# Kernel optimization log

Measured on AMD Instinct MI355X. Metric: run time of the kernel, lower is better.

The kernel has to match this reference:

```python
import jax, jax.numpy as jnp
import numpy as np

N_NODES = 50000
N_EDGES = 800000
IN_DIM = 256
HID_DIM = 128
N_LAYERS = 3


def setup_inputs() -> dict:
    key = jax.random.key(0)
    ks = jax.random.split(key, 7)
    s = 0.05
    x = jax.random.normal(ks[0], (N_NODES, IN_DIM), dtype=jnp.float32)
    edge_index = jax.random.randint(ks[1], (2, N_EDGES), 0, N_NODES, dtype=jnp.int64)
    W_enc = jax.random.normal(ks[2], (HID_DIM, IN_DIM), dtype=jnp.float32) * s
    b_enc = jax.random.normal(ks[3], (HID_DIM,), dtype=jnp.float32) * s
    W_l = jax.random.normal(ks[4], (N_LAYERS, HID_DIM, HID_DIM), dtype=jnp.float32) * s
    b_l = jax.random.normal(ks[5], (N_LAYERS, HID_DIM), dtype=jnp.float32) * s
    W_r = jax.random.normal(ks[6], (N_LAYERS, HID_DIM, HID_DIM), dtype=jnp.float32) * s
    return {"x": x, "edge_index": edge_index, "W_enc": W_enc, "b_enc": b_enc,
            "W_l": W_l, "b_l": b_l, "W_r": W_r}


def reference(x, edge_index, W_enc, b_enc, W_l, b_l, W_r):
    # eval mode: dropout is identity
    n = x.shape[0]
    src, dst = edge_index[0], edge_index[1]
    # encode: Linear(in_dim -> hid_dim)
    h = x @ W_enc.T + b_enc  # [N, H]
    # in-degree for mean aggregation (nodes with no in-edges -> 0 output)
    deg = jax.ops.segment_sum(jnp.ones((src.shape[0],), h.dtype), dst, num_segments=n)
    denom = jnp.maximum(deg, 1.0)[:, None]  # [N, 1]
    for i in range(W_l.shape[0]):
        # mean of source-node features over incoming edges
        agg = jax.ops.segment_sum(h[src], dst, num_segments=n) / denom  # [N, H]
        # SAGEConv: lin_l(agg) + lin_r(h)  (lin_r has no bias)
        h = agg @ W_l[i].T + b_l[i] + h @ W_r[i].T
    return h
```

## Files before the change

### kernel.cpp

```cpp
#include <hip/hip_runtime.h>

#define N_NODES 50000
#define N_EDGES 800000
#define IN_DIM 256
#define HID_DIM 128
#define ROWTILES (N_NODES / 16)
#define SCAT_BLOCKS (N_EDGES / 256)
#define ENC_BLOCKS 512
#define WCVT_BLOCKS 48
#define NBLK_LAYER 768
#define CAP_E 352

typedef float f4 __attribute__((ext_vector_type(4)));
typedef float f32x4 __attribute__((ext_vector_type(4)));
typedef float vf2 __attribute__((ext_vector_type(2)));
typedef short bf16x8 __attribute__((ext_vector_type(8)));

__device__ __forceinline__ unsigned short f2bf(float f) {
    unsigned u = __builtin_bit_cast(unsigned, f);
    return (unsigned short)((u + 0x7fffu + ((u >> 16) & 1u)) >> 16);
}
__device__ __forceinline__ unsigned pk2(float a, float b) {
    return (unsigned)f2bf(a) | ((unsigned)f2bf(b) << 16);
}
__device__ __forceinline__ bf16x8 cvt8(f4 a, f4 b) {
    union { bf16x8 v; unsigned u[4]; } r;
    r.u[0] = pk2(a[0], a[1]);
    r.u[1] = pk2(a[2], a[3]);
    r.u[2] = pk2(b[0], b[1]);
    r.u[3] = pk2(b[2], b[3]);
    return r.v;
}
__device__ __forceinline__ vf2 dec8(unsigned short t) {
    return __builtin_amdgcn_cvt_pk_f32_fp8((int)(unsigned)t, false);
}
__device__ __forceinline__ void gl_lds16(const void* g, void* l) {
    __builtin_amdgcn_global_load_lds(
        (const __attribute__((address_space(1))) unsigned int*)g,
        (__attribute__((address_space(3))) unsigned int*)l, 16, 0, 0);
}


__global__ __launch_bounds__(256) void k_pre(const int* __restrict__ src, const int* __restrict__ dst,
                                             int* __restrict__ tcnt16, unsigned* __restrict__ buf,
                                             const float* __restrict__ Wl, const float* __restrict__ Wr,
                                             unsigned short* __restrict__ wlrbf,
                                             const float* __restrict__ x,
                                             const float* __restrict__ Wenc,
                                             const float* __restrict__ bias,
                                             unsigned short* __restrict__ hout,
                                             unsigned char* __restrict__ f8out,
                                             int* __restrict__ ticket) {
    __shared__ float xs[2][4096];
    int tid = threadIdx.x;
    if (blockIdx.x < WCVT_BLOCKS) {
        int idx = blockIdx.x * 2048 + tid * 8;
        const float* srcp = (idx < 49152) ? (Wl + idx) : (Wr + (idx - 49152));
        const f4* g = (const f4*)srcp;
        *(bf16x8*)(wlrbf + idx) = cvt8(g[0], g[1]);
        return;
    }
    if (blockIdx.x >= WCVT_BLOCKS + ENC_BLOCKS) {
        int e = (blockIdx.x - WCVT_BLOCKS - ENC_BLOCKS) * 256 + tid;
        if (e < N_EDGES) {
            int sv = src[e], dv = dst[e];
            int t = dv >> 4, dl = dv & 15;
            int p = atomicAdd(&tcnt16[t * 16], 1);
            if (p < CAP_E) buf[t * CAP_E + p] = (unsigned)sv | ((unsigned)dl << 16);
        }
        return;
    }
    int bid = blockIdx.x - WCVT_BLOCKS;
    int lane = tid & 63;
    int wv = tid >> 6;
    int colbase = wv * 32;
    int lr = lane & 15;
    int kh = (lane >> 4) * 8;
    int khB = kh * 4;
    int swz = (lr & 7) << 4;

    bf16x8 bfr[2][8];
#pragma unroll
    for (int n = 0; n < 2; ++n) {
        const float* wp = Wenc + (size_t)(colbase + n * 16 + lr) * IN_DIM + kh;
#pragma unroll
        for (int s = 0; s < 8; ++s) {
            const f4* g = (const f4*)(wp + s * 32);
            bfr[n][s] = cvt8(g[0], g[1]);
        }
    }
    float bias0 = bias[colbase + lr];
    float bias1 = bias[colbase + 16 + lr];

    int pb = 0;
    for (int rt = bid; rt < ROWTILES; rt += ENC_BLOCKS, pb ^= 1) {
#pragma unroll
        for (int jj = 0; jj < 4; ++jj) {
            int j = wv * 4 + jj;
            const char* gsrc = (const char*)(x + (size_t)(rt * 16 + j) * IN_DIM)
                               + ((lane * 16) ^ ((j & 7) << 4));
            gl_lds16(gsrc, (char*)&xs[pb][0] + j * 1024);
        }
        __syncthreads();

        const char* xb = (const char*)&xs[pb][0] + lr * 1024;
        bf16x8 afr[8];
#pragma unroll
        for (int s = 0; s < 8; ++s) {
            int lo = khB + s * 128;
            f4 a = *(const f4*)(xb + ((lo) ^ swz));
            f4 b = *(const f4*)(xb + ((lo + 16) ^ swz));
            afr[s] = cvt8(a, b);
        }
        f32x4 acc0 = {0.f, 0.f, 0.f, 0.f}, acc1 = {0.f, 0.f, 0.f, 0.f};
#pragma unroll
        for (int s = 0; s < 8; ++s) {
            acc0 = __builtin_amdgcn_mfma_f32_16x16x32_bf16(afr[s], bfr[0][s], acc0, 0, 0, 0);
            acc1 = __builtin_amdgcn_mfma_f32_16x16x32_bf16(afr[s], bfr[1][s], acc1, 0, 0, 0);
        }
        int rbase = rt * 16 + (lane >> 4) * 4;
#pragma unroll
        for (int r = 0; r < 4; ++r) {
            float v0 = acc0[r] + bias0, v1 = acc1[r] + bias1;
            unsigned short* op = hout + (size_t)(rbase + r) * HID_DIM;
            op[colbase + lr] = f2bf(v0);
            op[colbase + 16 + lr] = f2bf(v1);
            unsigned pk = (unsigned)__builtin_amdgcn_cvt_pk_fp8_f32(v0, v1, 0, false);
            unsigned char* fp = f8out + (size_t)(rbase + r) * HID_DIM;
            fp[colbase + lr] = (unsigned char)(pk & 0xff);
            fp[colbase + 16 + lr] = (unsigned char)((pk >> 8) & 0xff);
        }
    }
    (void)ticket;
}


template <bool LAST>
__global__ __launch_bounds__(256) void k_layer(const unsigned short* __restrict__ H,
                                               const unsigned char* __restrict__ F8,
                                               const int* __restrict__ tcnt16,
                                               const unsigned* __restrict__ buf,
                                               const unsigned short* __restrict__ wlbf,
                                               const unsigned short* __restrict__ wrbf,
                                               const float* __restrict__ bias,
                                               unsigned short* __restrict__ hout,
                                               unsigned char* __restrict__ f8out,
                                               float* __restrict__ fout,
                                               int* __restrict__ ticket) {
    __shared__ unsigned char rowbuf[CAP_E * 128];
    __shared__ unsigned short sorted[CAP_E + 8];
    __shared__ unsigned short aggs[16][136];
    __shared__ int hist[16], pref[17], cur[16];
    __shared__ int tk;
    int tid = threadIdx.x;
    int lane = tid & 63;
    int wv = tid >> 6;
    int colbase = wv * 32;
    int lr = lane & 15;
    int kh = (lane >> 4) * 8;

    bf16x8 bl[2][4], br[2][4];
#pragma unroll
    for (int n = 0; n < 2; ++n) {
        const unsigned short* lp = wlbf + (size_t)(colbase + n * 16 + lr) * HID_DIM + kh;
        const unsigned short* rp = wrbf + (size_t)(colbase + n * 16 + lr) * HID_DIM + kh;
#pragma unroll
        for (int s = 0; s < 4; ++s) {
            bl[n][s] = *(const bf16x8*)(lp + s * 32);
            br[n][s] = *(const bf16x8*)(rp + s * 32);
        }
    }
    float bias0 = bias[colbase + lr];
    float bias1 = bias[colbase + 16 + lr];

    for (;;) {
        if (tid == 0) tk = atomicAdd(ticket, 1);
        if (tid < 16) hist[tid] = 0;
        __syncthreads();
        int rt = tk;
        if (rt >= ROWTILES) break;
        int cnt = tcnt16[rt * 16];
        cnt = (cnt > CAP_E) ? CAP_E : cnt;

        unsigned v0 = 0, v1 = 0;
        bool k0 = tid < cnt, k1 = tid + 256 < cnt;
        if (k0) v0 = buf[(size_t)rt * CAP_E + tid];
        if (k1) v1 = buf[(size_t)rt * CAP_E + tid + 256];
        if (k0) atomicAdd(&hist[v0 >> 16], 1);
        if (k1) atomicAdd(&hist[v1 >> 16], 1);
        __syncthreads();
        if (tid == 0) {
            int acc = 0;
#pragma unroll
            for (int q = 0; q < 16; ++q) { pref[q] = acc; cur[q] = acc; acc += hist[q]; }
            pref[16] = acc;
        }
        __syncthreads();
        if (k0) { int p = atomicAdd(&cur[v0 >> 16], 1); sorted[p] = (unsigned short)(v0 & 0xffff); }
        if (k1) { int p = atomicAdd(&cur[v1 >> 16], 1); sorted[p] = (unsigned short)(v1 & 0xffff); }
        __syncthreads();

        int rb0 = pref[wv * 4] >> 3;
        int rb1 = (pref[wv * 4 + 4] + 7) >> 3;
        for (int i = rb0; i < rb1; ++i) {
            int ee = i * 8 + (lane >> 3);
            ee = (ee > cnt - 1) ? cnt - 1 : ee;
            const unsigned char* gp = F8 + (size_t)sorted[ee] * HID_DIM + (lane & 7) * 16;
            gl_lds16(gp, &rowbuf[i * 1024]);
        }
        asm volatile("s_waitcnt vmcnt(0)" ::: "memory");
        __builtin_amdgcn_sched_barrier(0);

#pragma unroll
        for (int q = 0; q < 4; ++q) {
            int nq = wv * 4 + q;
            int jb = pref[nq], je = pref[nq + 1];
            float a0 = 0.f, a1 = 0.f;
            int j = jb;
            for (; j + 4 <= je; j += 4) {
                unsigned short t0 = *(const unsigned short*)&rowbuf[(j + 0) * 128 + lane * 2];
                unsigned short t1 = *(const unsigned short*)&rowbuf[(j + 1) * 128 + lane * 2];
                unsigned short t2 = *(const unsigned short*)&rowbuf[(j + 2) * 128 + lane * 2];
                unsigned short t3 = *(const unsigned short*)&rowbuf[(j + 3) * 128 + lane * 2];
                vf2 f0 = dec8(t0), f1 = dec8(t1), f2_ = dec8(t2), f3 = dec8(t3);
                a0 += (f0[0] + f1[0]) + (f2_[0] + f3[0]);
                a1 += (f0[1] + f1[1]) + (f2_[1] + f3[1]);
            }
            for (; j < je; ++j) {
                unsigned short t0 = *(const unsigned short*)&rowbuf[j * 128 + lane * 2];
                vf2 f0 = dec8(t0);
                a0 += f0[0];
                a1 += f0[1];
            }
            int dg = je - jb;
            float inv = 1.0f / (float)(dg > 0 ? dg : 1);
            *(unsigned*)&aggs[nq][lane * 2] = pk2(a0 * inv, a1 * inv);
        }
        __syncthreads();

        bf16x8 afr[4], hfr[4];
        const unsigned short* hp = H + (size_t)(rt * 16 + lr) * HID_DIM + kh;
#pragma unroll
        for (int s = 0; s < 4; ++s) {
            afr[s] = *(const bf16x8*)&aggs[lr][kh + s * 32];
            hfr[s] = *(const bf16x8*)(hp + s * 32);
        }
        f32x4 acc0 = {0.f, 0.f, 0.f, 0.f}, acc1 = {0.f, 0.f, 0.f, 0.f};
#pragma unroll
        for (int s = 0; s < 4; ++s) {
            acc0 = __builtin_amdgcn_mfma_f32_16x16x32_bf16(afr[s], bl[0][s], acc0, 0, 0, 0);
            acc1 = __builtin_amdgcn_mfma_f32_16x16x32_bf16(afr[s], bl[1][s], acc1, 0, 0, 0);
            acc0 = __builtin_amdgcn_mfma_f32_16x16x32_bf16(hfr[s], br[0][s], acc0, 0, 0, 0);
            acc1 = __builtin_amdgcn_mfma_f32_16x16x32_bf16(hfr[s], br[1][s], acc1, 0, 0, 0);
        }
        int rbase = rt * 16 + (lane >> 4) * 4;
#pragma unroll
        for (int r = 0; r < 4; ++r) {
            float v0 = acc0[r] + bias0, v1 = acc1[r] + bias1;
            if (LAST) {
                float* op = fout + (size_t)(rbase + r) * HID_DIM;
                op[colbase + lr] = v0;
                op[colbase + 16 + lr] = v1;
            } else {
                unsigned short* op = hout + (size_t)(rbase + r) * HID_DIM;
                op[colbase + lr] = f2bf(v0);
                op[colbase + 16 + lr] = f2bf(v1);
                unsigned pk = (unsigned)__builtin_amdgcn_cvt_pk_fp8_f32(v0, v1, 0, false);
                unsigned char* fp = f8out + (size_t)(rbase + r) * HID_DIM;
                fp[colbase + lr] = (unsigned char)(pk & 0xff);
                fp[colbase + 16 + lr] = (unsigned char)((pk >> 8) & 0xff);
            }
        }
    }
}


extern "C" void kernel_launch(void* const* d_in, const int* in_sizes, int n_in,
                              void* d_out, int out_size, void* d_ws, size_t ws_size,
                              hipStream_t stream) {
    const float* x    = (const float*)d_in[0];
    const int*   ei   = (const int*)d_in[1];
    const float* Wenc = (const float*)d_in[2];
    const float* benc = (const float*)d_in[3];
    const float* Wl   = (const float*)d_in[4];
    const float* bl   = (const float*)d_in[5];
    const float* Wr   = (const float*)d_in[6];
    float* out = (float*)d_out;

    const int* srcv = ei;
    const int* dstv = ei + N_EDGES;

    char* p = (char*)d_ws;
    unsigned short* h0    = (unsigned short*)p; p += (size_t)N_NODES * HID_DIM * 2;
    unsigned short* h1    = (unsigned short*)p; p += (size_t)N_NODES * HID_DIM * 2;
    unsigned char*  h0f   = (unsigned char*)p;  p += (size_t)N_NODES * HID_DIM;
    unsigned char*  h1f   = (unsigned char*)p;  p += (size_t)N_NODES * HID_DIM;
    unsigned short* wlrbf = (unsigned short*)p; p += 98304 * 2;
    int*      tcnt16 = (int*)p;      p += 3136 * 16 * 4;
    int*      tick   = (int*)p;      p += 256;
    unsigned* buf    = (unsigned*)p; p += (size_t)ROWTILES * CAP_E * 4;

    unsigned short* wlbf = wlrbf;
    unsigned short* wrbf = wlrbf + 49152;

    (void)hipMemsetAsync(tcnt16, 0, 3136 * 16 * 4 + 256, stream);
    k_pre<<<WCVT_BLOCKS + ENC_BLOCKS + SCAT_BLOCKS, 256, 0, stream>>>(
        srcv, dstv, tcnt16, buf, Wl, Wr, wlrbf, x, Wenc, benc, h0, h0f, tick);

    k_layer<false><<<NBLK_LAYER, 256, 0, stream>>>(h0, h0f, tcnt16, buf, wlbf, wrbf, bl,
                                                   h1, h1f, nullptr, tick + 1);
    k_layer<false><<<NBLK_LAYER, 256, 0, stream>>>(h1, h1f, tcnt16, buf, wlbf + 16384, wrbf + 16384,
                                                   bl + HID_DIM, h0, h0f, nullptr, tick + 2);
    k_layer<true><<<NBLK_LAYER, 256, 0, stream>>>(h0, h0f, tcnt16, buf, wlbf + 32768, wrbf + 32768,
                                                  bl + 2 * HID_DIM, nullptr, nullptr, out, tick + 3);
}
```

Measured before the change: 204.8 us.

## Replace global-atomic edge bucketing with count, prefix-scan and scatter passes

Edge bucketing by destination tile no longer uses one global atomic per edge. It now runs in three passes: per-chunk LDS histograms, a per-tile prefix scan across chunks, and a scatter pass that takes slots from LDS atomics. Global atomic contention goes away, and edges inside each tile keep a deterministic order by chunk. The cost is two extra kernel launches, plus count and offset matrices stored temporarily in the h1 buffer. The encoder block count is also raised from 512 to 1024.

```diff
diff --git a/kernel.cpp b/kernel.cpp
--- a/kernel.cpp
+++ b/kernel.cpp
@@ -4,12 +4,14 @@
 #define N_EDGES 800000
 #define IN_DIM 256
 #define HID_DIM 128
-#define ROWTILES (N_NODES / 16)
-#define SCAT_BLOCKS (N_EDGES / 256)
-#define ENC_BLOCKS 512
+#define ROWTILES 3125
+#define ENC_BLOCKS 1024
 #define WCVT_BLOCKS 48
+#define CNT_BLOCKS 256
+#define EDGES_PER_CB 3125
 #define NBLK_LAYER 768
 #define CAP_E 352
+#define TPAD 3136
 
 typedef float f4 __attribute__((ext_vector_type(4)));
 typedef float f32x4 __attribute__((ext_vector_type(4)));
@@ -41,17 +43,16 @@
 }
 
 
-__global__ __launch_bounds__(256) void k_pre(const int* __restrict__ src, const int* __restrict__ dst,
-                                             int* __restrict__ tcnt16, unsigned* __restrict__ buf,
+__global__ __launch_bounds__(256) void k_pre(const int* __restrict__ dst,
+                                             int* __restrict__ Cm,
                                              const float* __restrict__ Wl, const float* __restrict__ Wr,
                                              unsigned short* __restrict__ wlrbf,
                                              const float* __restrict__ x,
                                              const float* __restrict__ Wenc,
                                              const float* __restrict__ bias,
                                              unsigned short* __restrict__ hout,
-                                             unsigned char* __restrict__ f8out,
-                                             int* __restrict__ ticket) {
-    __shared__ float xs[2][4096];
+                                             unsigned char* __restrict__ f8out) {
+    __shared__ int smem_i[8192];
     int tid = threadIdx.x;
     if (blockIdx.x < WCVT_BLOCKS) {
         int idx = blockIdx.x * 2048 + tid * 8;
@@ -61,15 +62,19 @@
         return;
     }
     if (blockIdx.x >= WCVT_BLOCKS + ENC_BLOCKS) {
-        int e = (blockIdx.x - WCVT_BLOCKS - ENC_BLOCKS) * 256 + tid;
-        if (e < N_EDGES) {
-            int sv = src[e], dv = dst[e];
-            int t = dv >> 4, dl = dv & 15;
-            int p = atomicAdd(&tcnt16[t * 16], 1);
-            if (p < CAP_E) buf[t * CAP_E + p] = (unsigned)sv | ((unsigned)dl << 16);
-        }
+        int c = blockIdx.x - WCVT_BLOCKS - ENC_BLOCKS;
+        int* cnt = smem_i;
+        for (int i = tid; i < TPAD; i += 256) cnt[i] = 0;
+        __syncthreads();
+        const int* dp = dst + c * EDGES_PER_CB;
+        for (int i = tid; i < EDGES_PER_CB; i += 256)
+            atomicAdd(&cnt[dp[i] >> 4], 1);
+        __syncthreads();
+        int* crow = Cm + (size_t)c * TPAD;
+        for (int t = tid; t < TPAD; t += 256) crow[t] = cnt[t];
         return;
     }
+    float* xsf = (float*)smem_i;
     int bid = blockIdx.x - WCVT_BLOCKS;
     int lane = tid & 63;
     int wv = tid >> 6;
@@ -99,11 +104,11 @@
             int j = wv * 4 + jj;
             const char* gsrc = (const char*)(x + (size_t)(rt * 16 + j) * IN_DIM)
                                + ((lane * 16) ^ ((j & 7) << 4));
-            gl_lds16(gsrc, (char*)&xs[pb][0] + j * 1024);
-        }
-        __syncthreads();
-
-        const char* xb = (const char*)&xs[pb][0] + lr * 1024;
+            gl_lds16(gsrc, (char*)(xsf + pb * 4096) + j * 1024);
+        }
+        __syncthreads();
+
+        const char* xb = (const char*)(xsf + pb * 4096) + lr * 1024;
         bf16x8 afr[8];
 #pragma unroll
         for (int s = 0; s < 8; ++s) {
@@ -131,7 +136,56 @@
             fp[colbase + 16 + lr] = (unsigned char)((pk >> 8) & 0xff);
         }
     }
-    (void)ticket;
+}
+
+
+__global__ __launch_bounds__(256) void k_prefix(const int* __restrict__ Cm,
+                                                int* __restrict__ STm,
+                                                int* __restrict__ tcnt16) {
+    int tid = threadIdx.x;
+    int lane = tid & 63;
+    int t = blockIdx.x * 4 + (tid >> 6);
+    if (t >= ROWTILES) return;
+    int b0 = lane * 4;
+    int c0 = Cm[(size_t)(b0 + 0) * TPAD + t];
+    int c1 = Cm[(size_t)(b0 + 1) * TPAD + t];
+    int c2 = Cm[(size_t)(b0 + 2) * TPAD + t];
+    int c3 = Cm[(size_t)(b0 + 3) * TPAD + t];
+    int ls = c0 + c1 + c2 + c3;
+    int incl = ls;
+#pragma unroll
+    for (int off = 1; off < 64; off <<= 1) {
+        int v = __shfl_up(incl, off);
+        if (lane >= off) incl += v;
+    }
+    int excl = incl - ls;
+    STm[(size_t)(b0 + 0) * TPAD + t] = excl;
+    STm[(size_t)(b0 + 1) * TPAD + t] = excl + c0;
+    STm[(size_t)(b0 + 2) * TPAD + t] = excl + c0 + c1;
+    STm[(size_t)(b0 + 3) * TPAD + t] = excl + c0 + c1 + c2;
+    if (lane == 63) tcnt16[t * 16] = incl;
+}
+
+
+__global__ __launch_bounds__(256) void k_scat(const int* __restrict__ src, const int* __restrict__ dst,
+                                              const int* __restrict__ STm,
+                                              unsigned* __restrict__ buf) {
+    __shared__ int sbase[TPAD];
+    __shared__ int lcnt[TPAD];
+    int tid = threadIdx.x;
+    int c = blockIdx.x;
+    const int* strow = STm + (size_t)c * TPAD;
+    for (int i = tid; i < TPAD; i += 256) { sbase[i] = strow[i]; lcnt[i] = 0; }
+    __syncthreads();
+    const int* sp = src + c * EDGES_PER_CB;
+    const int* dp = dst + c * EDGES_PER_CB;
+    for (int i = tid; i < EDGES_PER_CB; i += 256) {
+        int sv = sp[i], dv = dp[i];
+        int t = dv >> 4, dl = dv & 15;
+        int r = atomicAdd(&lcnt[t], 1);
+        int slot = sbase[t] + r;
+        if (slot < CAP_E) buf[(size_t)t * CAP_E + slot] = (unsigned)sv | ((unsigned)dl << 16);
+    }
 }
 
 
@@ -300,12 +354,17 @@
     int*      tick   = (int*)p;      p += 256;
     unsigned* buf    = (unsigned*)p; p += (size_t)ROWTILES * CAP_E * 4;
 
+    int* Cm  = (int*)h1;
+    int* STm = (int*)((char*)h1 + (size_t)CNT_BLOCKS * TPAD * 4);
+
     unsigned short* wlbf = wlrbf;
     unsigned short* wrbf = wlrbf + 49152;
 
     (void)hipMemsetAsync(tcnt16, 0, 3136 * 16 * 4 + 256, stream);
-    k_pre<<<WCVT_BLOCKS + ENC_BLOCKS + SCAT_BLOCKS, 256, 0, stream>>>(
-        srcv, dstv, tcnt16, buf, Wl, Wr, wlrbf, x, Wenc, benc, h0, h0f, tick);
+    k_pre<<<WCVT_BLOCKS + ENC_BLOCKS + CNT_BLOCKS, 256, 0, stream>>>(
+        dstv, Cm, Wl, Wr, wlrbf, x, Wenc, benc, h0, h0f);
+    k_prefix<<<(ROWTILES + 3) / 4, 256, 0, stream>>>(Cm, STm, tcnt16);
+    k_scat<<<CNT_BLOCKS, 256, 0, stream>>>(srcv, dstv, STm, buf);
 
     k_layer<false><<<NBLK_LAYER, 256, 0, stream>>>(h0, h0f, tcnt16, buf, wlbf, wrbf, bl,
                                                    h1, h1f, nullptr, tick + 1);
```

Measured after the change: 215.1 us. +5.0%, slower.
